# Performance work log

Hardware: AMD Instinct MI355X
Metric: run time of the kernel (lower is better)

Reference implementation:

```python
import jax, jax.numpy as jnp
import numpy as np

N_NODES = 16384
N_EDGES = 65536
N_GRAPHS = 64


def setup_inputs() -> dict:
    key = jax.random.key(0)
    ks = iter(jax.random.split(key, 64))
    nk = lambda: next(ks)
    p = lambda *s: jax.random.normal(nk(), s, jnp.float32) * 0.1
    inp = {}
    inp['x'] = jax.random.normal(nk(), (N_NODES, 1), jnp.float32)
    inp['edge_index'] = jax.random.randint(nk(), (2, N_EDGES), 0, N_NODES, dtype=jnp.int32)
    inp['batch'] = jnp.sort(jax.random.randint(nk(), (N_NODES,), 0, N_GRAPHS, dtype=jnp.int32))
    for i, (fi, fo) in [(1, (1, 64)), (2, (64, 512)), (3, (512, 2048))]:
        inp[f'gat{i}_wl'] = p(fi, fo)
        inp[f'gat{i}_wr'] = p(fi, fo)
        inp[f'gat{i}_att'] = p(fo)
        inp[f'gat{i}_b'] = jnp.zeros((fo,), jnp.float32)
    for i, c in [(1, 64), (2, 512), (3, 2048), (4, 512), (5, 64)]:
        inp[f'gn{i}_w'] = jnp.ones((c,), jnp.float32)
        inp[f'gn{i}_b'] = jnp.zeros((c,), jnp.float32)
        inp[f'gn{i}_ms'] = jnp.ones((c,), jnp.float32)
    for i, (fi, fo) in [(1, (2048, 512)), (2, (512, 64))]:
        inp[f'arma{i}_wi'] = p(fi, fo)
        inp[f'arma{i}_wr'] = p(fi, fo)
        inp[f'arma{i}_b'] = jnp.zeros((fo,), jnp.float32)
    inp['lin_w'] = p(192, 2)
    inp['lin_b'] = jnp.zeros((2,), jnp.float32)
    return inp


def _seg_softmax(e, idx, n):
    m = jax.ops.segment_max(e, idx, num_segments=n)
    ex = jnp.exp(e - m[idx])
    s = jax.ops.segment_sum(ex, idx, num_segments=n)
    return ex / (s[idx] + 1e-16)


def _gatv2(x, src, dst, wl, wr, att, b):
    # GATv2: e_ij = a^T LeakyReLU(W_l x_j + W_r x_i), softmax over dst neighborhoods
    n = x.shape[0]
    xl = x @ wl
    xr = x @ wr
    e = jax.nn.leaky_relu(xl[src] + xr[dst], 0.2) @ att  # [E]
    a = _seg_softmax(e, dst, n)
    return jax.ops.segment_sum(xl[src] * a[:, None], dst, num_segments=n) + b


def _graph_norm(x, batch, w, b, ms, cnt):
    mean = jax.ops.segment_sum(x, batch, num_segments=N_GRAPHS) / cnt
    out = x - mean[batch] * ms
    var = jax.ops.segment_sum(out * out, batch, num_segments=N_GRAPHS) / cnt
    return w * out / jnp.sqrt(var + 1e-5)[batch] + b


def _arma(x, src, dst, norm, wi, wr, b):
    # ARMAConv, num_stacks=1, num_layers=1: ReLU(Ahat (x Wi) + x Wr + b)
    agg = jax.ops.segment_sum((x @ wi)[src] * norm[:, None], dst, num_segments=x.shape[0])
    return jax.nn.relu(agg + x @ wr + b)


def _forward(x, edge_index, batch,
             gat1_wl, gat1_wr, gat1_att, gat1_b, gn1_w, gn1_b, gn1_ms,
             gat2_wl, gat2_wr, gat2_att, gat2_b, gn2_w, gn2_b, gn2_ms,
             gat3_wl, gat3_wr, gat3_att, gat3_b, gn3_w, gn3_b, gn3_ms,
             arma1_wi, arma1_wr, arma1_b, gn4_w, gn4_b, gn4_ms,
             arma2_wi, arma2_wr, arma2_b, gn5_w, gn5_b, gn5_ms,
             lin_w, lin_b):
    n = x.shape[0]
    src, dst = edge_index[0], edge_index[1]
    sl = jnp.arange(n, dtype=edge_index.dtype)
    src_sl = jnp.concatenate([src, sl])  # GATv2 adds self loops
    dst_sl = jnp.concatenate([dst, sl])
    # gcn_norm without self loops (ARMAConv default)
    deg = jax.ops.segment_sum(jnp.ones_like(src, dtype=x.dtype), dst, num_segments=n)
    dis = jnp.where(deg > 0, 1.0 / jnp.sqrt(jnp.maximum(deg, 1.0)), 0.0)
    norm = dis[src] * dis[dst]
    cnt = jnp.maximum(jax.ops.segment_sum(jnp.ones((n,), x.dtype), batch, num_segments=N_GRAPHS), 1.0)[:, None]

    h = jax.nn.elu(_gatv2(x, src_sl, dst_sl, gat1_wl, gat1_wr, gat1_att, gat1_b))
    h = _graph_norm(h, batch, gn1_w, gn1_b, gn1_ms, cnt)
    h = jax.nn.elu(_gatv2(h, src_sl, dst_sl, gat2_wl, gat2_wr, gat2_att, gat2_b))
    h = _graph_norm(h, batch, gn2_w, gn2_b, gn2_ms, cnt)
    h = jax.nn.elu(_gatv2(h, src_sl, dst_sl, gat3_wl, gat3_wr, gat3_att, gat3_b))
    h = _graph_norm(h, batch, gn3_w, gn3_b, gn3_ms, cnt)
    h = jax.nn.elu(_arma(h, src, dst, norm, arma1_wi, arma1_wr, arma1_b))
    h = _graph_norm(h, batch, gn4_w, gn4_b, gn4_ms, cnt)
    h = jax.nn.elu(_arma(h, src, dst, norm, arma2_wi, arma2_wr, arma2_b))
    h = _graph_norm(h, batch, gn5_w, gn5_b, gn5_ms, cnt)

    x_max = jax.ops.segment_max(h, batch, num_segments=N_GRAPHS)
    x_sum = jax.ops.segment_sum(h, batch, num_segments=N_GRAPHS)
    x_mean = x_sum / cnt
    return jnp.concatenate([x_max, x_mean, x_sum], axis=1) @ lin_w + lin_b


def reference(x, edge_index, batch,
              gat1_wl, gat1_wr, gat1_att, gat1_b, gn1_w, gn1_b, gn1_ms,
              gat2_wl, gat2_wr, gat2_att, gat2_b, gn2_w, gn2_b, gn2_ms,
              gat3_wl, gat3_wr, gat3_att, gat3_b, gn3_w, gn3_b, gn3_ms,
              arma1_wi, arma1_wr, arma1_b, gn4_w, gn4_b, gn4_ms,
              arma2_wi, arma2_wr, arma2_b, gn5_w, gn5_b, gn5_ms,
              lin_w, lin_b):
    return _forward(x, edge_index, batch,
                    gat1_wl, gat1_wr, gat1_att, gat1_b, gn1_w, gn1_b, gn1_ms,
                    gat2_wl, gat2_wr, gat2_att, gat2_b, gn2_w, gn2_b, gn2_ms,
                    gat3_wl, gat3_wr, gat3_att, gat3_b, gn3_w, gn3_b, gn3_ms,
                    arma1_wi, arma1_wr, arma1_b, gn4_w, gn4_b, gn4_ms,
                    arma2_wi, arma2_wr, arma2_b, gn5_w, gn5_b, gn5_ms,
                    lin_w, lin_b)
```

## Files before the change

### kernel.cpp

```cpp
#include <hip/hip_runtime.h>
#include <hip/hip_bf16.h>

#define NN 16384
#define NE 65536
#define NESL (NE + NN)
#define NG 64

typedef __hip_bfloat16 bf16;
typedef __attribute__((ext_vector_type(8))) short short8v;
typedef __attribute__((ext_vector_type(4))) short short4v;
typedef __attribute__((ext_vector_type(4))) float f32x4;
typedef __attribute__((address_space(3))) void lds_void;
typedef const __attribute__((address_space(1))) void glb_void;

__device__ __forceinline__ short bfbits(float v) {
  bf16 h = __float2bfloat16(v);
  return *(short*)&h;
}
__device__ __forceinline__ float bfs2f(short s) {
  return __uint_as_float(((unsigned)(unsigned short)s) << 16);
}
__device__ __forceinline__ void gld16(const void* g, void* l) {
  __builtin_amdgcn_global_load_lds((glb_void*)g, (lds_void*)l, 16, 0, 0);
}

__global__ void k_zero2(int* a, int* b, int n) {
  int i = blockIdx.x * blockDim.x + threadIdx.x;
  if (i < n) { a[i] = 0; b[i] = 0; }
}


__global__ void k_ranges(const int* __restrict__ batch, int* __restrict__ R,
                         float* __restrict__ cnt) {
  int g = threadIdx.x;
  if (g <= NG) {
    int lo = 0, hi = NN;
    while (lo < hi) { int mid = (lo + hi) >> 1; if (batch[mid] < g) lo = mid + 1; else hi = mid; }
    R[g] = lo;
  }
  __syncthreads();
  if (g < NG) cnt[g] = fmaxf((float)(R[g + 1] - R[g]), 1.0f);
}

__global__ void k_deg(const int* __restrict__ dst, int* __restrict__ deg) {
  int e = blockIdx.x * blockDim.x + threadIdx.x;
  if (e < NE) atomicAdd(deg + dst[e], 1);
}

__global__ void k_dis(const int* __restrict__ deg, float* __restrict__ dis) {
  int n = blockIdx.x * blockDim.x + threadIdx.x;
  if (n < NN) { int d = deg[n]; dis[n] = d > 0 ? 1.0f / sqrtf((float)d) : 0.0f; }
}

__global__ void k_scan(const int* __restrict__ deg, int* __restrict__ rowptr) {
  __shared__ int sums[1024];
  int tid = threadIdx.x;
  int base = tid * 16;
  int loc[16];
  int run = 0;
#pragma unroll
  for (int i = 0; i < 16; i++) { run += deg[base + i] + 1; loc[i] = run; }
  sums[tid] = run;
  __syncthreads();
  for (int off = 1; off < 1024; off <<= 1) {
    int v = sums[tid];
    int u = (tid >= off) ? sums[tid - off] : 0;
    __syncthreads();
    sums[tid] = v + u;
    __syncthreads();
  }
  int offset = (tid > 0) ? sums[tid - 1] : 0;
  if (tid == 0) rowptr[0] = 0;
#pragma unroll
  for (int i = 0; i < 16; i++) rowptr[base + i + 1] = loc[i] + offset;
}

__global__ void k_fill(const int* __restrict__ src, const int* __restrict__ dst,
                       const int* __restrict__ rowptr, const float* __restrict__ dis,
                       int* __restrict__ fill, int* __restrict__ srck,
                       float* __restrict__ normk) {
  int e = blockIdx.x * blockDim.x + threadIdx.x;
  if (e >= NESL) return;
  int s = e < NE ? src[e] : e - NE;
  int d = e < NE ? dst[e] : e - NE;
  int pos = rowptr[d] + atomicAdd(fill + d, 1);
  srck[pos] = s;
  normk[pos] = e < NE ? dis[s] * dis[d] : 0.0f;
}

__global__ void k_wsplit2(const float* __restrict__ wa, const float* __restrict__ wb,
                          short* __restrict__ hi, short* __restrict__ lo, int K, int Nw) {
  int gi = blockIdx.x * blockDim.x + threadIdx.x;
  int ngroups = (Nw >> 6) * (K >> 5) * 512;
  if (gi >= ngroups) return;
  int g = gi & 511;
  int t = gi >> 9;
  int nkb = K >> 5;
  int tn = t / nkb, tk = t % nkb;
  int lane = g & 63;
  int n = tn * 128 + ((g >> 6) << 4) + (lane & 15);
  int kb = tk * 32 + ((lane >> 4) << 3);
  const float* w = (n < Nw) ? wa : wb;
  int nn = (n < Nw) ? n : n - Nw;
  short8v h, l;
#pragma unroll
  for (int j = 0; j < 8; j++) {
    float v = w[(size_t)(kb + j) * Nw + nn];
    short hb = bfbits(v);
    h[j] = hb;
    l[j] = bfbits(v - bfs2f(hb));
  }
  *(short8v*)(hi + (size_t)gi * 8) = h;
  *(short8v*)(lo + (size_t)gi * 8) = l;
}

template <int SPLITA, int CBF16, int ACT>
__global__ __launch_bounds__(256) void gemm_mfma_p(const short* __restrict__ Ahi,
                                                   const short* __restrict__ Alo,
                                                   const short* __restrict__ Bthi,
                                                   const short* __restrict__ Btlo,
                                                   void* __restrict__ Cp,
                                                   const float* __restrict__ bias,
                                                   int M, int N, int K) {
  __shared__ __align__(16) short sA[2][(SPLITA ? 2 : 1) * 4096];
  __shared__ __align__(16) short sB[2][8192];
  const int tid = threadIdx.x;
  const int wave = tid >> 6, lane = tid & 63;
  const int wm = wave >> 1, wn = wave & 1;
  const int nbx = gridDim.x;
  const int nwg = nbx * gridDim.y;
  const int hw = blockIdx.y * nbx + blockIdx.x;
  const int lg = (hw & 7) * (nwg >> 3) + (hw >> 3);
  const int row0 = (lg / nbx) * 128, col0 = (lg % nbx) * 128;
  const int nkb = K >> 5;
  const int c = wave * 2;
  const int ar = lane & 15, akc = lane >> 4;
  f32x4 acc[4][4] = {};

  auto stage = [&](int buf, int kb) {
    const short* bh = Bthi + ((size_t)(col0 >> 7) * nkb + kb) * 4096;
    const short* bl = Btlo + ((size_t)(col0 >> 7) * nkb + kb) * 4096;
    gld16(bh + (size_t)c * 512 + lane * 8, (char*)sB[buf] + c * 1024);
    gld16(bh + (size_t)(c + 1) * 512 + lane * 8, (char*)sB[buf] + (c + 1) * 1024);
    gld16(bl + (size_t)c * 512 + lane * 8, (char*)sB[buf] + 8192 + c * 1024);
    gld16(bl + (size_t)(c + 1) * 512 + lane * 8, (char*)sB[buf] + 8192 + (c + 1) * 1024);
    gld16(Ahi + (size_t)(row0 + c * 16 + ar) * K + kb * 32 + akc * 8,
          (char*)sA[buf] + c * 1024);
    gld16(Ahi + (size_t)(row0 + (c + 1) * 16 + ar) * K + kb * 32 + akc * 8,
          (char*)sA[buf] + (c + 1) * 1024);
    if constexpr (SPLITA) {
      gld16(Alo + (size_t)(row0 + c * 16 + ar) * K + kb * 32 + akc * 8,
            (char*)sA[buf] + 8192 + c * 1024);
      gld16(Alo + (size_t)(row0 + (c + 1) * 16 + ar) * K + kb * 32 + akc * 8,
            (char*)sA[buf] + 8192 + (c + 1) * 1024);
    }
  };

  stage(0, 0);
  for (int kb = 0; kb < nkb; kb++) {
    int cur = kb & 1;
    if (kb + 1 < nkb) {
      stage(cur ^ 1, kb + 1);
      if constexpr (SPLITA)
        asm volatile("s_waitcnt vmcnt(8)" ::: "memory");
      else
        asm volatile("s_waitcnt vmcnt(6)" ::: "memory");
    } else {
      asm volatile("s_waitcnt vmcnt(0)" ::: "memory");
    }
    __builtin_amdgcn_sched_barrier(0);
    __builtin_amdgcn_s_barrier();
    __builtin_amdgcn_sched_barrier(0);
    asm volatile("" ::: "memory");
    short8v af[4], al[4], bh[4], bl[4];
#pragma unroll
    for (int f = 0; f < 4; f++) {
      af[f] = *(short8v*)((char*)sA[cur] + (wm * 4 + f) * 1024 + lane * 16);
      if constexpr (SPLITA)
        al[f] = *(short8v*)((char*)sA[cur] + 8192 + (wm * 4 + f) * 1024 + lane * 16);
      bh[f] = *(short8v*)((char*)sB[cur] + (wn * 4 + f) * 1024 + lane * 16);
      bl[f] = *(short8v*)((char*)sB[cur] + 8192 + (wn * 4 + f) * 1024 + lane * 16);
    }
#pragma unroll
    for (int i = 0; i < 4; i++)
#pragma unroll
      for (int j = 0; j < 4; j++) {
        acc[i][j] = __builtin_amdgcn_mfma_f32_16x16x32_bf16(af[i], bh[j], acc[i][j], 0, 0, 0);
        acc[i][j] = __builtin_amdgcn_mfma_f32_16x16x32_bf16(af[i], bl[j], acc[i][j], 0, 0, 0);
        if constexpr (SPLITA)
          acc[i][j] = __builtin_amdgcn_mfma_f32_16x16x32_bf16(al[i], bh[j], acc[i][j], 0, 0, 0);
      }
    asm volatile("" ::: "memory");
    __builtin_amdgcn_sched_barrier(0);
    __builtin_amdgcn_s_barrier();
    __builtin_amdgcn_sched_barrier(0);
  }
#pragma unroll
  for (int i = 0; i < 4; i++)
#pragma unroll
    for (int j = 0; j < 4; j++)
#pragma unroll
      for (int r = 0; r < 4; r++) {
        int row = row0 + wm * 64 + i * 16 + ((lane >> 4) << 2) + r;
        int col = col0 + wn * 64 + j * 16 + (lane & 15);
        float v = acc[i][j][r];
        if (bias) v += bias[col];
        if constexpr (ACT == 1) v = v > 0.0f ? v : expf(v) - 1.0f;
        if constexpr (ACT == 2) v = fmaxf(v, 0.0f);
        if constexpr (CBF16) {
          ((short*)Cp)[(size_t)row * N + col] = bfbits(v);
        } else {
          ((float*)Cp)[(size_t)row * N + col] = v;
        }
      }
}

template <int CBF16, int ACT>
__global__ __launch_bounds__(512) void gemm_mfma_p256(const short* __restrict__ Ahi,
                                                      const short* __restrict__ Bthi,
                                                      const short* __restrict__ Btlo,
                                                      void* __restrict__ Cp,
                                                      const float* __restrict__ bias,
                                                      int M, int N, int K) {
  __shared__ __align__(16) short sA[2][8192];
  __shared__ __align__(16) short sB[2][8192];
  const int tid = threadIdx.x;
  const int wave = tid >> 6, lane = tid & 63;
  const int wm = wave >> 1, wn = wave & 1;
  const int nbx = gridDim.x;
  const int nwg = nbx * gridDim.y;
  const int hw = blockIdx.y * nbx + blockIdx.x;
  const int lg = (hw & 7) * (nwg >> 3) + (hw >> 3);
  const int row0 = (lg / nbx) * 256, col0 = (lg % nbx) * 128;
  const int nkb = K >> 5;
  const int ar = lane & 15, akc = lane >> 4;
  f32x4 acc[4][4] = {};

  auto stage = [&](int buf, int kb) {
    if (wave < 4) {
      const short* bh = Bthi + ((size_t)(col0 >> 7) * nkb + kb) * 4096;
      int cB = wave * 2;
      gld16(bh + (size_t)cB * 512 + lane * 8, (char*)sB[buf] + cB * 1024);
      gld16(bh + (size_t)(cB + 1) * 512 + lane * 8, (char*)sB[buf] + (cB + 1) * 1024);
    } else {
      const short* bl = Btlo + ((size_t)(col0 >> 7) * nkb + kb) * 4096;
      int cB = (wave - 4) * 2;
      gld16(bl + (size_t)cB * 512 + lane * 8, (char*)sB[buf] + 8192 + cB * 1024);
      gld16(bl + (size_t)(cB + 1) * 512 + lane * 8, (char*)sB[buf] + 8192 + (cB + 1) * 1024);
    }
    int cA = wave * 2;
    gld16(Ahi + (size_t)(row0 + cA * 16 + ar) * K + kb * 32 + akc * 8,
          (char*)sA[buf] + cA * 1024);
    gld16(Ahi + (size_t)(row0 + (cA + 1) * 16 + ar) * K + kb * 32 + akc * 8,
          (char*)sA[buf] + (cA + 1) * 1024);
  };

  stage(0, 0);
  for (int kb = 0; kb < nkb; kb++) {
    int cur = kb & 1;
    if (kb + 1 < nkb) {
      stage(cur ^ 1, kb + 1);
      asm volatile("s_waitcnt vmcnt(4)" ::: "memory");
    } else {
      asm volatile("s_waitcnt vmcnt(0)" ::: "memory");
    }
    __builtin_amdgcn_sched_barrier(0);
    __builtin_amdgcn_s_barrier();
    __builtin_amdgcn_sched_barrier(0);
    asm volatile("" ::: "memory");
    short8v af[4], bh[4], bl[4];
#pragma unroll
    for (int f = 0; f < 4; f++) {
      af[f] = *(short8v*)((char*)sA[cur] + (wm * 4 + f) * 1024 + lane * 16);
      bh[f] = *(short8v*)((char*)sB[cur] + (wn * 4 + f) * 1024 + lane * 16);
      bl[f] = *(short8v*)((char*)sB[cur] + 8192 + (wn * 4 + f) * 1024 + lane * 16);
    }
#pragma unroll
    for (int i = 0; i < 4; i++)
#pragma unroll
      for (int j = 0; j < 4; j++) {
        acc[i][j] = __builtin_amdgcn_mfma_f32_16x16x32_bf16(af[i], bh[j], acc[i][j], 0, 0, 0);
        acc[i][j] = __builtin_amdgcn_mfma_f32_16x16x32_bf16(af[i], bl[j], acc[i][j], 0, 0, 0);
      }
    asm volatile("" ::: "memory");
    __builtin_amdgcn_sched_barrier(0);
    __builtin_amdgcn_s_barrier();
    __builtin_amdgcn_sched_barrier(0);
  }
#pragma unroll
  for (int i = 0; i < 4; i++)
#pragma unroll
    for (int j = 0; j < 4; j++)
#pragma unroll
      for (int r = 0; r < 4; r++) {
        int row = row0 + wm * 64 + i * 16 + ((lane >> 4) << 2) + r;
        int col = col0 + wn * 64 + j * 16 + (lane & 15);
        float v = acc[i][j][r];
        if (bias) v += bias[col];
        if constexpr (ACT == 1) v = v > 0.0f ? v : expf(v) - 1.0f;
        if constexpr (ACT == 2) v = fmaxf(v, 0.0f);
        if constexpr (CBF16) {
          ((short*)Cp)[(size_t)row * N + col] = bfbits(v);
        } else {
          ((float*)Cp)[(size_t)row * N + col] = v;
        }
      }
}

__global__ void k_gat1_csr(const float* __restrict__ x, const float* __restrict__ wl,
                           const float* __restrict__ wr, const float* __restrict__ att,
                           const int* __restrict__ rowptr, const int* __restrict__ srck,
                           float* __restrict__ ework, const float* __restrict__ bias,
                           float* __restrict__ out) {
  int node = blockIdx.x * 4 + (threadIdx.x >> 6);
  int lane = threadIdx.x & 63;
  float wlv = wl[lane], wrv = wr[lane], av = att[lane];
  float xd = x[node];
  int beg = rowptr[node], end = rowptr[node + 1];
  float m = -INFINITY;
  for (int k = beg; k < end; k++) {
    float v = x[srck[k]] * wlv + xd * wrv;
    v = v > 0.0f ? v : 0.2f * v;
    float e = av * v;
#pragma unroll
    for (int off = 32; off; off >>= 1) e += __shfl_xor(e, off);
    if (lane == 0) ework[k] = e;
    m = fmaxf(m, e);
  }
  __syncthreads();
  float sum = 0.0f, agg = 0.0f;
  for (int k = beg + lane; k < end; k += 64) {
    float p = expf(ework[k] - m);
    sum += p;
    agg += p * x[srck[k]];
  }
#pragma unroll
  for (int off = 32; off; off >>= 1) {
    sum += __shfl_xor(sum, off);
    agg += __shfl_xor(agg, off);
  }
  float o = agg / (sum + 1e-16f) * wlv + bias[lane];
  out[(size_t)node * 64 + lane] = o > 0.0f ? o : expf(o) - 1.0f;
}

template <int FO, int STR, typename XT>
__global__ void k_logits_csr(const XT* __restrict__ X, const float* __restrict__ att,
                             const int* __restrict__ rowptr, const int* __restrict__ srck,
                             float* __restrict__ pk, float* __restrict__ ssum) {
  int node = blockIdx.x * 4 + (threadIdx.x >> 6);
  int lane = threadIdx.x & 63;
  constexpr int NV = FO / 64;
  float xr[NV], at[NV];
  if constexpr (sizeof(XT) == 2) {
    const short* xrp = (const short*)X + (size_t)node * STR + FO;
#pragma unroll
    for (int j = 0; j < FO / 512; j++) {
      short8v v = *(const short8v*)(xrp + j * 512 + lane * 8);
      f32x4 a0 = *(const f32x4*)(att + j * 512 + lane * 8);
      f32x4 a1 = *(const f32x4*)(att + j * 512 + lane * 8 + 4);
#pragma unroll
      for (int t = 0; t < 8; t++) {
        xr[j * 8 + t] = bfs2f(v[t]);
        at[j * 8 + t] = t < 4 ? a0[t] : a1[t - 4];
      }
    }
  } else {
    const float* xrp = (const float*)X + (size_t)node * STR + FO;
#pragma unroll
    for (int j = 0; j < FO / 256; j++) {
      f32x4 v = *(const f32x4*)(xrp + j * 256 + lane * 4);
      f32x4 a = *(const f32x4*)(att + j * 256 + lane * 4);
#pragma unroll
      for (int t = 0; t < 4; t++) {
        xr[j * 4 + t] = v[t];
        at[j * 4 + t] = a[t];
      }
    }
  }
  int beg = rowptr[node], end = rowptr[node + 1];
  float m = -INFINITY;
  for (int k = beg; k < end; k++) {
    int s = srck[k];
    float acc = 0.0f;
    if constexpr (sizeof(XT) == 2) {
      const short* xlp = (const short*)X + (size_t)s * STR;
#pragma unroll
      for (int j = 0; j < FO / 512; j++) {
        short8v v = *(const short8v*)(xlp + j * 512 + lane * 8);
#pragma unroll
        for (int t = 0; t < 8; t++) {
          float u = bfs2f(v[t]) + xr[j * 8 + t];
          u = u > 0.0f ? u : 0.2f * u;
          acc += at[j * 8 + t] * u;
        }
      }
    } else {
      const float* xlp = (const float*)X + (size_t)s * STR;
#pragma unroll
      for (int j = 0; j < FO / 256; j++) {
        f32x4 v = *(const f32x4*)(xlp + j * 256 + lane * 4);
#pragma unroll
        for (int t = 0; t < 4; t++) {
          float u = v[t] + xr[j * 4 + t];
          u = u > 0.0f ? u : 0.2f * u;
          acc += at[j * 4 + t] * u;
        }
      }
    }
#pragma unroll
    for (int off = 32; off; off >>= 1) acc += __shfl_xor(acc, off);
    if (lane == 0) pk[k] = acc;
    m = fmaxf(m, acc);
  }
  __syncthreads();
  float sum = 0.0f;
  for (int k = beg + lane; k < end; k += 64) {
    float p = expf(pk[k] - m);
    pk[k] = p;
    sum += p;
  }
#pragma unroll
  for (int off = 32; off; off >>= 1) sum += __shfl_xor(sum, off);
  if (lane == 0) ssum[node] = sum;
}

template <int MODE, int SSTR, int OSTR>
__global__ void k_agg512(const float* __restrict__ Xsrc, const float* __restrict__ pk,
                         const float* __restrict__ ssum, const int* __restrict__ rowptr,
                         const int* __restrict__ srck, const float* __restrict__ normk,
                         const float* __restrict__ xwrb, const float* __restrict__ bias,
                         float* __restrict__ out, short* __restrict__ outhi,
                         short* __restrict__ outlo) {
  int wave = threadIdx.x >> 6;
  int node = blockIdx.x * 2 + (wave >> 1);
  int lane = threadIdx.x & 63;
  int c0 = (wave & 1) * 256 + lane * 4;
  f32x4 acc = {};
  int beg = rowptr[node], end = rowptr[node + 1];
  float inv = (MODE == 0) ? 1.0f / (ssum[node] + 1e-16f) : 1.0f;
  for (int k = beg; k < end; k++) {
    int s = srck[k];
    float w = (MODE == 0) ? pk[k] * inv : normk[k];
    f32x4 v = *(const f32x4*)(Xsrc + (size_t)s * SSTR + c0);
#pragma unroll
    for (int t = 0; t < 4; t++) acc[t] += w * v[t];
  }
  if constexpr (MODE == 1) {
    f32x4 xv = *(const f32x4*)(xwrb + (size_t)node * SSTR + 512 + c0);
#pragma unroll
    for (int t = 0; t < 4; t++) acc[t] = fmaxf(acc[t] + xv[t] + bias[c0 + t], 0.0f);
    *(f32x4*)(out + (size_t)node * OSTR + c0) = acc;
  } else {
    short4v hh, ll;
#pragma unroll
    for (int t = 0; t < 4; t++) {
      hh[t] = bfbits(acc[t]);
      ll[t] = bfbits(acc[t] - bfs2f(hh[t]));
    }
    *(short4v*)(outhi + (size_t)node * OSTR + c0) = hh;
    *(short4v*)(outlo + (size_t)node * OSTR + c0) = ll;
  }
}

template <int MODE, int SSTR, int XOFF>
__global__ void k_agg64(const float* __restrict__ Xsrc, const float* __restrict__ pk,
                        const float* __restrict__ ssum, const int* __restrict__ rowptr,
                        const int* __restrict__ srck, const float* __restrict__ normk,
                        const float* __restrict__ xwrb, const float* __restrict__ bias,
                        float* __restrict__ out, short* __restrict__ outhi,
                        short* __restrict__ outlo) {
  int node = blockIdx.x * (blockDim.x >> 6) + (threadIdx.x >> 6);
  if (node >= NN) return;
  int lane = threadIdx.x & 63;
  int cg = lane & 15, eg = lane >> 4;
  int c0 = cg * 4;
  f32x4 acc = {};
  int beg = rowptr[node], end = rowptr[node + 1];
  float inv = (MODE == 0) ? 1.0f / (ssum[node] + 1e-16f) : 1.0f;
  for (int k = beg + eg; k < end; k += 4) {
    int s = srck[k];
    float w = (MODE == 0) ? pk[k] * inv : normk[k];
    f32x4 v = *(const f32x4*)(Xsrc + (size_t)s * SSTR + c0);
#pragma unroll
    for (int t = 0; t < 4; t++) acc[t] += w * v[t];
  }
#pragma unroll
  for (int t = 0; t < 4; t++) {
    acc[t] += __shfl_xor(acc[t], 16);
    acc[t] += __shfl_xor(acc[t], 32);
  }
  if (eg == 0) {
    if constexpr (MODE == 1) {
      f32x4 xv = *(const f32x4*)(xwrb + (size_t)node * SSTR + XOFF + c0);
#pragma unroll
      for (int t = 0; t < 4; t++) acc[t] = fmaxf(acc[t] + xv[t] + bias[c0 + t], 0.0f);
      *(f32x4*)(out + (size_t)node * 64 + c0) = acc;
    } else {
      short4v hh, ll;
#pragma unroll
      for (int t = 0; t < 4; t++) {
        hh[t] = bfbits(acc[t]);
        ll[t] = bfbits(acc[t] - bfs2f(hh[t]));
      }
      *(short4v*)(outhi + (size_t)node * 64 + c0) = hh;
      *(short4v*)(outlo + (size_t)node * 64 + c0) = ll;
    }
  }
}

template <typename T, int VEC>
__global__ void k_gn_stats_v(const T* __restrict__ x, const int* __restrict__ R, int C,
                             float* __restrict__ s1p, float* __restrict__ s2p) {
  int g = blockIdx.x;
  int rs = blockIdx.y;
  int RS = gridDim.y;
  int c0 = threadIdx.x * VEC;
  if (c0 >= C) return;
  int beg = R[g], end = R[g + 1];
  int len = end - beg;
  int lo = beg + (int)(((long long)len * rs) / RS);
  int hi2 = beg + (int)(((long long)len * (rs + 1)) / RS);
  float a[VEC] = {}, b[VEC] = {};
  for (int n = lo; n < hi2; n++) {
    const T* p = x + (size_t)n * C + c0;
    float v[VEC];
    if constexpr (sizeof(T) == 2) {
      short8v h = *(const short8v*)p;
#pragma unroll
      for (int t = 0; t < VEC; t++) v[t] = bfs2f(h[t]);
    } else {
      f32x4 h = *(const f32x4*)p;
#pragma unroll
      for (int t = 0; t < VEC; t++) v[t] = h[t];
    }
#pragma unroll
    for (int t = 0; t < VEC; t++) {
      a[t] += v[t];
      b[t] += v[t] * v[t];
    }
  }
#pragma unroll
  for (int t = 0; t < VEC; t++) {
    s1p[((size_t)rs * NG + g) * C + c0 + t] = a[t];
    s2p[((size_t)rs * NG + g) * C + c0 + t] = b[t];
  }
}

template <typename T, int VEC, int EMIT>
__global__ void k_gn_apply_v(T* __restrict__ x, const int* __restrict__ batch,
                             const float* __restrict__ cnt, const float* __restrict__ s1p,
                             const float* __restrict__ s2p, const float* __restrict__ w,
                             const float* __restrict__ b, const float* __restrict__ ms, int C,
                             int total_vec, short* __restrict__ hip,
                             short* __restrict__ lop) {
  int i = blockIdx.x * blockDim.x + threadIdx.x;
  if (i >= total_vec) return;
  int cpv = C / VEC;
  int n = i / cpv, c0 = (i % cpv) * VEC;
  int g = batch[n];
  float ct = cnt[g];
  T* p = x + (size_t)n * C + c0;
  float v[VEC];
  if constexpr (sizeof(T) == 2) {
    short8v h = *(const short8v*)p;
#pragma unroll
    for (int t = 0; t < VEC; t++) v[t] = bfs2f(h[t]);
  } else {
    f32x4 h = *(const f32x4*)p;
#pragma unroll
    for (int t = 0; t < VEC; t++) v[t] = h[t];
  }
#pragma unroll
  for (int t = 0; t < VEC; t++) {
    int cc = c0 + t;
    float sv1 = 0.0f, sv2 = 0.0f;
#pragma unroll
    for (int rs = 0; rs < 4; rs++) {
      sv1 += s1p[((size_t)rs * NG + g) * C + cc];
      sv2 += s2p[((size_t)rs * NG + g) * C + cc];
    }
    float mean = sv1 / ct;
    float mm = mean * ms[cc];
    float var = sv2 / ct - 2.0f * mm * mean + mm * mm;
    v[t] = (v[t] - mm) * (1.0f / sqrtf(var + 1e-5f)) * w[cc] + b[cc];
  }
  if constexpr (sizeof(T) == 2) {
    short8v h;
#pragma unroll
    for (int t = 0; t < VEC; t++) h[t] = bfbits(v[t]);
    *(short8v*)p = h;
  } else {
    f32x4 h;
#pragma unroll
    for (int t = 0; t < VEC; t++) h[t] = v[t];
    *(f32x4*)p = h;
  }
  if constexpr (EMIT >= 2) {
    short4v hh;
#pragma unroll
    for (int t = 0; t < VEC; t++) hh[t] = bfbits(v[t]);
    *(short4v*)(hip + (size_t)n * C + c0) = hh;
    if constexpr (EMIT == 3) {
      short4v ll;
#pragma unroll
      for (int t = 0; t < VEC; t++) ll[t] = bfbits(v[t] - bfs2f(hh[t]));
      *(short4v*)(lop + (size_t)n * C + c0) = ll;
    }
  }
}

__global__ void k_pool(const float* __restrict__ h, const int* __restrict__ R,
                       const float* __restrict__ cnt, const float* __restrict__ lw,
                       const float* __restrict__ lb, float* __restrict__ out) {
  int g = blockIdx.x;
  int c = threadIdx.x;
  int beg = R[g], end = R[g + 1];
  float mx = -INFINITY, sm = 0.0f;
  for (int n = beg; n < end; n++) {
    float v = h[(size_t)n * 64 + c];
    mx = fmaxf(mx, v);
    sm += v;
  }
  __shared__ float feat[192];
  feat[c] = mx;
  feat[64 + c] = sm / cnt[g];
  feat[128 + c] = sm;
  __syncthreads();
  if (c < 2) {
    float acc = lb[c];
    for (int j = 0; j < 192; j++) acc += feat[j] * lw[j * 2 + c];
    out[g * 2 + c] = acc;
  }
}


extern "C" void kernel_launch(void* const* d_in, const int* in_sizes, int n_in,
                              void* d_out, int out_size, void* d_ws, size_t ws_size,
                              hipStream_t stream) {
  const float* x = (const float*)d_in[0];
  const int* ei = (const int*)d_in[1];
  const int* batch = (const int*)d_in[2];
  const float* g1wl = (const float*)d_in[3];
  const float* g1wr = (const float*)d_in[4];
  const float* g1att = (const float*)d_in[5];
  const float* g1b = (const float*)d_in[6];
  const float* g2wl = (const float*)d_in[7];
  const float* g2wr = (const float*)d_in[8];
  const float* g2att = (const float*)d_in[9];
  const float* g2b = (const float*)d_in[10];
  const float* g3wl = (const float*)d_in[11];
  const float* g3wr = (const float*)d_in[12];
  const float* g3att = (const float*)d_in[13];
  const float* g3b = (const float*)d_in[14];
  const float* gn1w = (const float*)d_in[15];
  const float* gn1b = (const float*)d_in[16];
  const float* gn1ms = (const float*)d_in[17];
  const float* gn2w = (const float*)d_in[18];
  const float* gn2b = (const float*)d_in[19];
  const float* gn2ms = (const float*)d_in[20];
  const float* gn3w = (const float*)d_in[21];
  const float* gn3b = (const float*)d_in[22];
  const float* gn3ms = (const float*)d_in[23];
  const float* gn4w = (const float*)d_in[24];
  const float* gn4b = (const float*)d_in[25];
  const float* gn4ms = (const float*)d_in[26];
  const float* gn5w = (const float*)d_in[27];
  const float* gn5b = (const float*)d_in[28];
  const float* gn5ms = (const float*)d_in[29];
  const float* a1wi = (const float*)d_in[30];
  const float* a1wr = (const float*)d_in[31];
  const float* a1b = (const float*)d_in[32];
  const float* a2wi = (const float*)d_in[33];
  const float* a2wr = (const float*)d_in[34];
  const float* a2b = (const float*)d_in[35];
  const float* linw = (const float*)d_in[36];
  const float* linb = (const float*)d_in[37];
  const int* srcp = ei;
  const int* dstp = ei + NE;
  float* out = (float*)d_out;

  float* ws = (float*)d_ws;
  size_t o = 0;
  auto alloc = [&](size_t nfloats) { float* p = ws + o; o += nfloats; return p; };
  float* BIG0f = alloc((size_t)NN * 1024);
  float* BIG1f = alloc((size_t)NN * 1024);
  float* B0 = alloc((size_t)NN * 512);
  float* B1 = alloc((size_t)NN * 512);
  float* h1 = alloc((size_t)NN * 64);
  float* S0 = alloc((size_t)NN * 64);
  float* S1 = alloc((size_t)NN * 64);
  float* S2 = alloc((size_t)NN * 64);
  float* pk = alloc(NESL);
  float* normk = alloc(NESL);
  float* ssum = alloc(NN);
  float* dis = alloc(NN);
  float* cnt = alloc(NG);
  float* s1 = alloc((size_t)4 * NG * 2048);
  float* s2 = alloc((size_t)4 * NG * 2048);
  short* WThi = (short*)alloc((size_t)4096 * 512 / 2);
  short* WTlo = (short*)alloc((size_t)4096 * 512 / 2);
  int* deg = (int*)alloc(NN);
  int* rowptr = (int*)alloc(NN + 1);
  int* fill = (int*)alloc(NN);
  int* srck = (int*)alloc(NESL);
  int* R = (int*)alloc(72);

  bf16* XLR3 = (bf16*)BIG0f;
  bf16* h3 = (bf16*)BIG0f;
  float* h4 = BIG1f;
  short* h4hi = (short*)BIG0f;
  short* h4lo = h4hi + (size_t)NN * 512;
  short* XLR2 = (short*)B0;
  float* h2 = B0;
  short* h2hi = (short*)B1;
  short* agg2hi = (short*)B1;
  short* agg2lo = agg2hi + (size_t)NN * 512;
  float* TXW1 = B0;
  float* TXW2 = S0;
  short* h1hi = (short*)S2;
  short* h1lo = h1hi + (size_t)NN * 64;
  short* aggShi = (short*)S0;
  short* aggSlo = aggShi + (size_t)NN * 64;
  float* h5 = S2;

  k_zero2<<<NN / 256, 256, 0, stream>>>(deg, fill, NN);
  k_ranges<<<1, 128, 0, stream>>>(batch, R, cnt);
  k_deg<<<NE / 256, 256, 0, stream>>>(dstp, deg);
  k_scan<<<1, 1024, 0, stream>>>(deg, rowptr);
  k_dis<<<NN / 256, 256, 0, stream>>>(deg, dis);
  k_fill<<<(NESL + 255) / 256, 256, 0, stream>>>(srcp, dstp, rowptr, dis, fill, srck, normk);

  k_gat1_csr<<<NN / 4, 256, 0, stream>>>(x, g1wl, g1wr, g1att, rowptr, srck, pk, g1b, h1);
  k_gn_stats_v<float, 4><<<dim3(NG, 4), 16, 0, stream>>>(h1, R, 64, s1, s2);
  k_gn_apply_v<float, 4, 3><<<NN * 16 / 256, 256, 0, stream>>>(h1, batch, cnt, s1, s2, gn1w,
                                                               gn1b, gn1ms, 64, NN * 16, h1hi,
                                                               h1lo);

  k_wsplit2<<<8192 / 256, 256, 0, stream>>>(g2wl, g2wr, WThi, WTlo, 64, 512);
  gemm_mfma_p<1, 1, 0><<<dim3(8, 128), 256, 0, stream>>>(h1hi, h1lo, WThi, WTlo, XLR2, nullptr,
                                                         NN, 1024, 64);
  k_logits_csr<512, 1024, bf16><<<NN / 4, 256, 0, stream>>>((const bf16*)XLR2, g2att, rowptr,
                                                            srck, pk, ssum);
  k_agg64<0, 64, 0><<<NN / 4, 256, 0, stream>>>(h1, pk, ssum, rowptr, srck, normk, nullptr,
                                                nullptr, nullptr, aggShi, aggSlo);
  gemm_mfma_p<1, 0, 1><<<dim3(4, 128), 256, 0, stream>>>(aggShi, aggSlo, WThi, WTlo, h2, g2b,
                                                         NN, 512, 64);
  k_gn_stats_v<float, 4><<<dim3(NG, 4), 128, 0, stream>>>(h2, R, 512, s1, s2);
  k_gn_apply_v<float, 4, 2><<<NN * 128 / 256, 256, 0, stream>>>(h2, batch, cnt, s1, s2, gn2w,
                                                                gn2b, gn2ms, 512, NN * 128,
                                                                h2hi, nullptr);

  k_wsplit2<<<262144 / 256, 256, 0, stream>>>(g3wl, g3wr, WThi, WTlo, 512, 2048);
  gemm_mfma_p256<1, 0><<<dim3(32, 64), 512, 0, stream>>>(h2hi, WThi, WTlo, XLR3, nullptr, NN,
                                                         4096, 512);
  k_logits_csr<2048, 4096, bf16><<<NN / 4, 256, 0, stream>>>(XLR3, g3att, rowptr, srck, pk, ssum);
  k_agg512<0, 512, 512><<<NN / 2, 256, 0, stream>>>(h2, pk, ssum, rowptr, srck, normk, nullptr,
                                                    nullptr, nullptr, agg2hi, agg2lo);
  gemm_mfma_p<1, 1, 1><<<dim3(16, 128), 256, 0, stream>>>(agg2hi, agg2lo, WThi, WTlo, h3, g3b,
                                                          NN, 2048, 512);
  k_gn_stats_v<bf16, 8><<<dim3(NG, 4), 256, 0, stream>>>(h3, R, 2048, s1, s2);
  k_gn_apply_v<bf16, 8, 0><<<NN * 256 / 256, 256, 0, stream>>>(h3, batch, cnt, s1, s2, gn3w,
                                                               gn3b, gn3ms, 2048, NN * 256,
                                                               nullptr, nullptr);

  k_wsplit2<<<262144 / 256, 256, 0, stream>>>(a1wi, a1wr, WThi, WTlo, 2048, 512);
  gemm_mfma_p256<0, 0><<<dim3(8, 64), 512, 0, stream>>>((const short*)h3, WThi, WTlo, TXW1,
                                                        nullptr, NN, 1024, 2048);
  k_agg512<1, 1024, 512><<<NN / 2, 256, 0, stream>>>(TXW1, pk, nullptr, rowptr, srck, normk,
                                                     TXW1, a1b, h4, nullptr, nullptr);
  k_gn_stats_v<float, 4><<<dim3(NG, 4), 128, 0, stream>>>(h4, R, 512, s1, s2);
  k_gn_apply_v<float, 4, 3><<<NN * 128 / 256, 256, 0, stream>>>(h4, batch, cnt, s1, s2, gn4w,
                                                                gn4b, gn4ms, 512, NN * 128,
                                                                h4hi, h4lo);

  k_wsplit2<<<8192 / 256, 256, 0, stream>>>(a2wi, a2wr, WThi, WTlo, 512, 64);
  gemm_mfma_p<1, 0, 0><<<dim3(1, 128), 256, 0, stream>>>(h4hi, h4lo, WThi, WTlo, TXW2, nullptr,
                                                         NN, 128, 512);
  k_agg64<1, 128, 64><<<NN / 4, 256, 0, stream>>>(TXW2, pk, nullptr, rowptr, srck, normk, TXW2,
                                                  a2b, h5, nullptr, nullptr);
  k_gn_stats_v<float, 4><<<dim3(NG, 4), 16, 0, stream>>>(h5, R, 64, s1, s2);
  k_gn_apply_v<float, 4, 0><<<NN * 16 / 256, 256, 0, stream>>>(h5, batch, cnt, s1, s2, gn5w,
                                                               gn5b, gn5ms, 64, NN * 16, nullptr,
                                                               nullptr);

  k_pool<<<NG, 64, 0, stream>>>(h5, R, cnt, linw, linb, out);
}
```

Baseline: 1.102 ms.

## Store GAT3 output as bf16 hi/lo pair and use split-A GEMM for ARMA1

The GAT3 output h3 was stored as plain bf16 and fed to a single-bf16-A 256-wide GEMM. It is now stored as a hi/lo bf16 pair, with new graph-norm stats and apply kernels that work on the pair. The ARMA1 GEMM (K=2048) switches to the split-A 128-tile kernel, which runs MFMAs on both the hi and lo parts of A. This raises accuracy but doubles A traffic and adds MFMA work on the largest GEMM. It also doubles the bytes the norm kernels read and write, so the change looks driven by accuracy rather than speed.

```diff
diff --git a/kernel.cpp b/kernel.cpp
--- a/kernel.cpp
+++ b/kernel.cpp
@@ -114,12 +114,13 @@
   *(short8v*)(lo + (size_t)gi * 8) = l;
 }
 
-template <int SPLITA, int CBF16, int ACT>
+template <int SPLITA, int COUT, int ACT>
 __global__ __launch_bounds__(256) void gemm_mfma_p(const short* __restrict__ Ahi,
                                                    const short* __restrict__ Alo,
                                                    const short* __restrict__ Bthi,
                                                    const short* __restrict__ Btlo,
                                                    void* __restrict__ Cp,
+                                                   short* __restrict__ Clo,
                                                    const float* __restrict__ bias,
                                                    int M, int N, int K) {
   __shared__ __align__(16) short sA[2][(SPLITA ? 2 : 1) * 4096];
@@ -207,8 +208,12 @@
         if (bias) v += bias[col];
         if constexpr (ACT == 1) v = v > 0.0f ? v : expf(v) - 1.0f;
         if constexpr (ACT == 2) v = fmaxf(v, 0.0f);
-        if constexpr (CBF16) {
+        if constexpr (COUT == 1) {
           ((short*)Cp)[(size_t)row * N + col] = bfbits(v);
+        } else if constexpr (COUT == 2) {
+          short hb = bfbits(v);
+          ((short*)Cp)[(size_t)row * N + col] = hb;
+          Clo[(size_t)row * N + col] = bfbits(v - bfs2f(hb));
         } else {
           ((float*)Cp)[(size_t)row * N + col] = v;
         }
@@ -546,6 +551,72 @@
   }
 }
 
+__global__ void k_gn_stats_pair(const short* __restrict__ xhi, const short* __restrict__ xlo,
+                                const int* __restrict__ R, int C, float* __restrict__ s1p,
+                                float* __restrict__ s2p) {
+  int g = blockIdx.x;
+  int rs = blockIdx.y;
+  int RS = gridDim.y;
+  int c0 = threadIdx.x * 8;
+  if (c0 >= C) return;
+  int beg = R[g], end = R[g + 1];
+  int len = end - beg;
+  int lo = beg + (int)(((long long)len * rs) / RS);
+  int hi2 = beg + (int)(((long long)len * (rs + 1)) / RS);
+  float a[8] = {}, b[8] = {};
+  for (int n = lo; n < hi2; n++) {
+    short8v h = *(const short8v*)(xhi + (size_t)n * C + c0);
+    short8v l = *(const short8v*)(xlo + (size_t)n * C + c0);
+#pragma unroll
+    for (int t = 0; t < 8; t++) {
+      float v = bfs2f(h[t]) + bfs2f(l[t]);
+      a[t] += v;
+      b[t] += v * v;
+    }
+  }
+#pragma unroll
+  for (int t = 0; t < 8; t++) {
+    s1p[((size_t)rs * NG + g) * C + c0 + t] = a[t];
+    s2p[((size_t)rs * NG + g) * C + c0 + t] = b[t];
+  }
+}
+
+__global__ void k_gn_apply_pair(short* __restrict__ xhi, short* __restrict__ xlo,
+                                const int* __restrict__ batch, const float* __restrict__ cnt,
+                                const float* __restrict__ s1p, const float* __restrict__ s2p,
+                                const float* __restrict__ w, const float* __restrict__ b,
+                                const float* __restrict__ ms, int C, int total_vec) {
+  int i = blockIdx.x * blockDim.x + threadIdx.x;
+  if (i >= total_vec) return;
+  int cpv = C / 8;
+  int n = i / cpv, c0 = (i % cpv) * 8;
+  int g = batch[n];
+  float ct = cnt[g];
+  short8v h = *(const short8v*)(xhi + (size_t)n * C + c0);
+  short8v l = *(const short8v*)(xlo + (size_t)n * C + c0);
+  short8v ho, loo;
+#pragma unroll
+  for (int t = 0; t < 8; t++) {
+    int cc = c0 + t;
+    float sv1 = 0.0f, sv2 = 0.0f;
+#pragma unroll
+    for (int rs = 0; rs < 4; rs++) {
+      sv1 += s1p[((size_t)rs * NG + g) * C + cc];
+      sv2 += s2p[((size_t)rs * NG + g) * C + cc];
+    }
+    float mean = sv1 / ct;
+    float mm = mean * ms[cc];
+    float var = sv2 / ct - 2.0f * mm * mean + mm * mm;
+    float v = bfs2f(h[t]) + bfs2f(l[t]);
+    v = (v - mm) * (1.0f / sqrtf(var + 1e-5f)) * w[cc] + b[cc];
+    short hb = bfbits(v);
+    ho[t] = hb;
+    loo[t] = bfbits(v - bfs2f(hb));
+  }
+  *(short8v*)(xhi + (size_t)n * C + c0) = ho;
+  *(short8v*)(xlo + (size_t)n * C + c0) = loo;
+}
+
 template <typename T, int VEC, int EMIT>
 __global__ void k_gn_apply_v(T* __restrict__ x, const int* __restrict__ batch,
                              const float* __restrict__ cnt, const float* __restrict__ s1p,
@@ -595,7 +666,7 @@
     for (int t = 0; t < VEC; t++) h[t] = v[t];
     *(f32x4*)p = h;
   }
-  if constexpr (EMIT >= 2) {
+  if constexpr (EMIT == 2 || EMIT == 3) {
     short4v hh;
 #pragma unroll
     for (int t = 0; t < VEC; t++) hh[t] = bfbits(v[t]);
@@ -706,7 +777,8 @@
   int* R = (int*)alloc(72);
 
   bf16* XLR3 = (bf16*)BIG0f;
-  bf16* h3 = (bf16*)BIG0f;
+  short* h3hi = (short*)BIG0f;
+  short* h3lo = (short*)BIG1f;
   float* h4 = BIG1f;
   short* h4hi = (short*)BIG0f;
   short* h4lo = h4hi + (size_t)NN * 512;
@@ -738,13 +810,13 @@
 
   k_wsplit2<<<8192 / 256, 256, 0, stream>>>(g2wl, g2wr, WThi, WTlo, 64, 512);
   gemm_mfma_p<1, 1, 0><<<dim3(8, 128), 256, 0, stream>>>(h1hi, h1lo, WThi, WTlo, XLR2, nullptr,
-                                                         NN, 1024, 64);
+                                                         nullptr, NN, 1024, 64);
   k_logits_csr<512, 1024, bf16><<<NN / 4, 256, 0, stream>>>((const bf16*)XLR2, g2att, rowptr,
                                                             srck, pk, ssum);
   k_agg64<0, 64, 0><<<NN / 4, 256, 0, stream>>>(h1, pk, ssum, rowptr, srck, normk, nullptr,
                                                 nullptr, nullptr, aggShi, aggSlo);
-  gemm_mfma_p<1, 0, 1><<<dim3(4, 128), 256, 0, stream>>>(aggShi, aggSlo, WThi, WTlo, h2, g2b,
-                                                         NN, 512, 64);
+  gemm_mfma_p<1, 0, 1><<<dim3(4, 128), 256, 0, stream>>>(aggShi, aggSlo, WThi, WTlo, h2,
+                                                         nullptr, g2b, NN, 512, 64);
   k_gn_stats_v<float, 4><<<dim3(NG, 4), 128, 0, stream>>>(h2, R, 512, s1, s2);
   k_gn_apply_v<float, 4, 2><<<NN * 128 / 256, 256, 0, stream>>>(h2, batch, cnt, s1, s2, gn2w,
                                                                 gn2b, gn2ms, 512, NN * 128,
@@ -756,16 +828,15 @@
   k_logits_csr<2048, 4096, bf16><<<NN / 4, 256, 0, stream>>>(XLR3, g3att, rowptr, srck, pk, ssum);
   k_agg512<0, 512, 512><<<NN / 2, 256, 0, stream>>>(h2, pk, ssum, rowptr, srck, normk, nullptr,
                                                     nullptr, nullptr, agg2hi, agg2lo);
-  gemm_mfma_p<1, 1, 1><<<dim3(16, 128), 256, 0, stream>>>(agg2hi, agg2lo, WThi, WTlo, h3, g3b,
-                                                          NN, 2048, 512);
-  k_gn_stats_v<bf16, 8><<<dim3(NG, 4), 256, 0, stream>>>(h3, R, 2048, s1, s2);
-  k_gn_apply_v<bf16, 8, 0><<<NN * 256 / 256, 256, 0, stream>>>(h3, batch, cnt, s1, s2, gn3w,
-                                                               gn3b, gn3ms, 2048, NN * 256,
-                                                               nullptr, nullptr);
+  gemm_mfma_p<1, 2, 1><<<dim3(16, 128), 256, 0, stream>>>(agg2hi, agg2lo, WThi, WTlo, h3hi,
+                                                          h3lo, g3b, NN, 2048, 512);
+  k_gn_stats_pair<<<dim3(NG, 4), 256, 0, stream>>>(h3hi, h3lo, R, 2048, s1, s2);
+  k_gn_apply_pair<<<NN * 256 / 256, 256, 0, stream>>>(h3hi, h3lo, batch, cnt, s1, s2, gn3w,
+                                                      gn3b, gn3ms, 2048, NN * 256);
 
   k_wsplit2<<<262144 / 256, 256, 0, stream>>>(a1wi, a1wr, WThi, WTlo, 2048, 512);
-  gemm_mfma_p256<0, 0><<<dim3(8, 64), 512, 0, stream>>>((const short*)h3, WThi, WTlo, TXW1,
-                                                        nullptr, NN, 1024, 2048);
+  gemm_mfma_p<1, 0, 0><<<dim3(8, 128), 256, 0, stream>>>(h3hi, h3lo, WThi, WTlo, TXW1, nullptr,
+                                                         nullptr, NN, 1024, 2048);
   k_agg512<1, 1024, 512><<<NN / 2, 256, 0, stream>>>(TXW1, pk, nullptr, rowptr, srck, normk,
                                                      TXW1, a1b, h4, nullptr, nullptr);
   k_gn_stats_v<float, 4><<<dim3(NG, 4), 128, 0, stream>>>(h4, R, 512, s1, s2);
@@ -775,7 +846,7 @@
 
   k_wsplit2<<<8192 / 256, 256, 0, stream>>>(a2wi, a2wr, WThi, WTlo, 512, 64);
   gemm_mfma_p<1, 0, 0><<<dim3(1, 128), 256, 0, stream>>>(h4hi, h4lo, WThi, WTlo, TXW2, nullptr,
-                                                         NN, 128, 512);
+                                                         nullptr, NN, 128, 512);
   k_agg64<1, 128, 64><<<NN / 4, 256, 0, stream>>>(TXW2, pk, nullptr, rowptr, srck, normk, TXW2,
                                                   a2b, h5, nullptr, nullptr);
   k_gn_stats_v<float, 4><<<dim3(NG, 4), 16, 0, stream>>>(h5, R, 64, s1, s2);
```

Result: slower. 1.146 ms (+4.0%).
